# Optimization experiments

Hardware: AMD Instinct MI355X
Metric: run time of the kernel (lower is better)

## Reference

```python
import jax, jax.numpy as jnp
import numpy as np
from jax import lax

MAX_DISP = 4
KERNEL = 2 * MAX_DISP + 1  # 9
PAD = MAX_DISP             # 4


def setup_inputs() -> dict:
    key = jax.random.key(0)
    k1, k2 = jax.random.split(key)
    B, C, H, W = 4096, 512, 4, 4
    feat1 = jax.random.normal(k1, (B, C, H, W), dtype=jnp.float32)
    feat2 = jax.random.normal(k2, (B, C, H, W), dtype=jnp.float32)
    return {"feat1": feat1, "feat2": feat2}


def reference(feat1, feat2):
    # feat1, feat2: [B, C, 4, 4]
    B, C, H, W = feat1.shape
    # F.pad(feat2, [4]*4) -> [B, C, 12, 12], then crop rows/cols 2:11 -> 9x9 kernel
    feat2_pad = jnp.pad(feat2, ((0, 0), (0, 0), (PAD, PAD), (PAD, PAD)))
    feat2_crop = feat2_pad[:, :, 2:2 + KERNEL, 2:2 + KERNEL]  # [B, C, 9, 9]
    weight = feat2_crop.reshape(B * C, 1, KERNEL, KERNEL)     # OIHW, groups=B*C
    inp = feat1.reshape(1, B * C, H, W)                       # NCHW
    # torch F.conv2d is cross-correlation; lax conv is too (no kernel flip)
    corr = lax.conv_general_dilated(
        inp, weight,
        window_strides=(1, 1),
        padding=[(PAD, PAD), (PAD, PAD)],
        dimension_numbers=("NCHW", "OIHW", "NCHW"),
        feature_group_count=B * C,
    )  # [1, B*C, 4, 4]
    corr = corr.reshape(B, C, H, W)
    return corr.sum(axis=1, keepdims=True)  # [B, 1, 4, 4]
```

## Files before the change

kernel.cpp:

```cpp
#include <hip/hip_runtime.h>


__global__ __launch_bounds__(256, 4) void corr_kernel(
        const float4* __restrict__ feat1,
        const float4* __restrict__ feat2,
        float* __restrict__ out, int B) {
    const int lane  = threadIdx.x & 63;
    const int wid   = blockIdx.x * 4 + (threadIdx.x >> 6);
    const int nwave = gridDim.x * 4;

    for (int b = wid; b < B; b += nwave) {
        const size_t bbase = (size_t)b * 512;

        float4 A[2][4], W[2][4];
        {
            const size_t idx = (bbase + lane) * 4;
            #pragma unroll
            for (int i = 0; i < 4; ++i) { A[0][i] = feat1[idx + i]; W[0][i] = feat2[idx + i]; }
        }

        float acc[16];
        #pragma unroll
        for (int i = 0; i < 16; ++i) acc[i] = 0.f;

        #pragma unroll
        for (int k = 0; k < 8; ++k) {
            const int cur = k & 1, nxt = cur ^ 1;
            if (k < 7) {
                const size_t idx = (bbase + (size_t)(k + 1) * 64 + lane) * 4;
                #pragma unroll
                for (int i = 0; i < 4; ++i) { A[nxt][i] = feat1[idx + i]; W[nxt][i] = feat2[idx + i]; }
            }
            __builtin_amdgcn_sched_barrier(0);

            const float a[16] = { A[cur][0].x, A[cur][0].y, A[cur][0].z, A[cur][0].w,
                                  A[cur][1].x, A[cur][1].y, A[cur][1].z, A[cur][1].w,
                                  A[cur][2].x, A[cur][2].y, A[cur][2].z, A[cur][2].w,
                                  A[cur][3].x, A[cur][3].y, A[cur][3].z, A[cur][3].w };
            const float w[16] = { W[cur][0].x, W[cur][0].y, W[cur][0].z, W[cur][0].w,
                                  W[cur][1].x, W[cur][1].y, W[cur][1].z, W[cur][1].w,
                                  W[cur][2].x, W[cur][2].y, W[cur][2].z, W[cur][2].w,
                                  W[cur][3].x, W[cur][3].y, W[cur][3].z, W[cur][3].w };

            #pragma unroll
            for (int y = 0; y < 4; ++y)
            #pragma unroll
            for (int p = 0; p < 4; ++p) {
                const int u = y + p - 2;
                if (u < 0 || u > 3) continue;
                #pragma unroll
                for (int x = 0; x < 4; ++x)
                #pragma unroll
                for (int q = 0; q < 4; ++q) {
                    const int v = x + q - 2;
                    if (v < 0 || v > 3) continue;
                    acc[y*4 + x] = fmaf(a[u*4 + v], w[p*4 + q], acc[y*4 + x]);
                }
            }
        }

        float v[16];
        #pragma unroll
        for (int i = 0; i < 16; ++i) v[i] = acc[i];
        #pragma unroll
        for (int k = 0; k < 4; ++k) {
            const int m = 1 << k;
            const int pairs = 8 >> k;
            const bool sel = (lane >> k) & 1;
            float wtmp[8];
            #pragma unroll
            for (int p = 0; p < pairs; ++p) {
                float keep = sel ? v[2*p+1] : v[2*p];
                float send = sel ? v[2*p]   : v[2*p+1];
                float recv = __shfl_xor(send, m, 64);
                wtmp[p] = keep + recv;
            }
            #pragma unroll
            for (int p = 0; p < pairs; ++p) v[p] = wtmp[p];
        }
        float r = v[0];
        r += __shfl_xor(r, 16, 64);
        r += __shfl_xor(r, 32, 64);

        if (lane < 16) out[(size_t)b * 16 + lane] = r;
    }
}

extern "C" void kernel_launch(void* const* d_in, const int* in_sizes, int n_in,
                              void* d_out, int out_size, void* d_ws, size_t ws_size,
                              hipStream_t stream) {
    const float4* feat1 = (const float4*)d_in[0];
    const float4* feat2 = (const float4*)d_in[1];
    float* out = (float*)d_out;
    const int B = in_sizes[0] / (512 * 16);
    const int blocks = (B + 3) / 4;
    corr_kernel<<<dim3(blocks), dim3(256), 0, stream>>>(feat1, feat2, out, B);
}
```

Baseline: 271.3 us.

## Split each channel's 4x4 map across lanes using row shuffles, two waves per batch

Each lane now loads one float4 row of a channel instead of a whole 4x4 map, so lanes read consecutive 16-byte rows (coalesced). Other rows of feat2 come in through xor shuffles, cutting per-lane FMAs and register use. Each batch element is split across two waves that combine partials through shared memory, and occupancy rises to 6 blocks. This adds shuffle traffic, a block-level sync, a lane-dependent remap step before the reduction, and drops the bounds check on B.

```diff
diff --git a/kernel.cpp b/kernel.cpp
--- a/kernel.cpp
+++ b/kernel.cpp
@@ -1,88 +1,112 @@
 #include <hip/hip_runtime.h>
 
 
-__global__ __launch_bounds__(256, 4) void corr_kernel(
+__device__ __forceinline__ float4 shflx4(float4 v, int m) {
+    float4 r;
+    r.x = __shfl_xor(v.x, m, 64);
+    r.y = __shfl_xor(v.y, m, 64);
+    r.z = __shfl_xor(v.z, m, 64);
+    r.w = __shfl_xor(v.w, m, 64);
+    return r;
+}
+
+__global__ __launch_bounds__(256, 6) void corr_kernel(
         const float4* __restrict__ feat1,
         const float4* __restrict__ feat2,
-        float* __restrict__ out, int B) {
-    const int lane  = threadIdx.x & 63;
-    const int wid   = blockIdx.x * 4 + (threadIdx.x >> 6);
-    const int nwave = gridDim.x * 4;
+        float* __restrict__ out) {
+    const int tid  = threadIdx.x;
+    const int lane = tid & 63;
+    const int wv   = tid >> 6;
+    const int bsub = wv >> 1;
+    const int half = wv & 1;
+    const int b    = blockIdx.x * 2 + bsub;
+    const int u    = lane & 3;
 
-    for (int b = wid; b < B; b += nwave) {
-        const size_t bbase = (size_t)b * 512;
+    const size_t kbase = (size_t)b * 2048 + (size_t)half * 1024 + lane;
 
-        float4 A[2][4], W[2][4];
-        {
-            const size_t idx = (bbase + lane) * 4;
-            #pragma unroll
-            for (int i = 0; i < 4; ++i) { A[0][i] = feat1[idx + i]; W[0][i] = feat2[idx + i]; }
+    float racc[4][4];
+    #pragma unroll
+    for (int t = 0; t < 4; ++t)
+        #pragma unroll
+        for (int x = 0; x < 4; ++x) racc[t][x] = 0.f;
+
+    float4 Abuf[2], Wbuf[2];
+    Abuf[0] = feat1[kbase];
+    Wbuf[0] = feat2[kbase];
+
+    #pragma unroll
+    for (int j = 0; j < 16; ++j) {
+        const int cur = j & 1, nxt = cur ^ 1;
+        if (j < 15) {
+            Abuf[nxt] = feat1[kbase + (size_t)(j + 1) * 64];
+            Wbuf[nxt] = feat2[kbase + (size_t)(j + 1) * 64];
         }
+        __builtin_amdgcn_sched_barrier(0);
 
-        float acc[16];
-        #pragma unroll
-        for (int i = 0; i < 16; ++i) acc[i] = 0.f;
+        const float4 Av = Abuf[cur];
+        const float4 w0 = Wbuf[cur];
+        const float4 w1 = shflx4(w0, 1);
+        const float4 w2 = shflx4(w0, 2);
+        const float4 w3 = shflx4(w0, 3);
+
+        const float a[4] = {Av.x, Av.y, Av.z, Av.w};
+        const float wr[4][4] = {
+            {w0.x, w0.y, w0.z, w0.w},
+            {w1.x, w1.y, w1.z, w1.w},
+            {w2.x, w2.y, w2.z, w2.w},
+            {w3.x, w3.y, w3.z, w3.w}};
 
         #pragma unroll
-        for (int k = 0; k < 8; ++k) {
-            const int cur = k & 1, nxt = cur ^ 1;
-            if (k < 7) {
-                const size_t idx = (bbase + (size_t)(k + 1) * 64 + lane) * 4;
+        for (int t = 0; t < 4; ++t)
+            #pragma unroll
+            for (int x = 0; x < 4; ++x)
                 #pragma unroll
-                for (int i = 0; i < 4; ++i) { A[nxt][i] = feat1[idx + i]; W[nxt][i] = feat2[idx + i]; }
-            }
-            __builtin_amdgcn_sched_barrier(0);
+                for (int kk = 0; kk < 4; ++kk) {
+                    const int v = x + kk - 2;
+                    if (v < 0 || v > 3) continue;
+                    racc[t][x] = fmaf(a[v], wr[t][kk], racc[t][x]);
+                }
+    }
 
-            const float a[16] = { A[cur][0].x, A[cur][0].y, A[cur][0].z, A[cur][0].w,
-                                  A[cur][1].x, A[cur][1].y, A[cur][1].z, A[cur][1].w,
-                                  A[cur][2].x, A[cur][2].y, A[cur][2].z, A[cur][2].w,
-                                  A[cur][3].x, A[cur][3].y, A[cur][3].z, A[cur][3].w };
-            const float w[16] = { W[cur][0].x, W[cur][0].y, W[cur][0].z, W[cur][0].w,
-                                  W[cur][1].x, W[cur][1].y, W[cur][1].z, W[cur][1].w,
-                                  W[cur][2].x, W[cur][2].y, W[cur][2].z, W[cur][2].w,
-                                  W[cur][3].x, W[cur][3].y, W[cur][3].z, W[cur][3].w };
+    float v16[16];
+    #pragma unroll
+    for (int x = 0; x < 4; ++x) {
+        v16[2 * 4 + x] = racc[0][x];
+        v16[1 * 4 + x] = (u == 0 || u == 2) ? racc[1][x]
+                        : (u == 1 ? racc[3][x] : 0.f);
+        v16[3 * 4 + x] = (u == 1 || u == 3) ? racc[1][x]
+                        : (u == 2 ? racc[3][x] : 0.f);
+        v16[0 * 4 + x] = (u < 2) ? racc[2][x] : 0.f;
+    }
 
-            #pragma unroll
-            for (int y = 0; y < 4; ++y)
-            #pragma unroll
-            for (int p = 0; p < 4; ++p) {
-                const int u = y + p - 2;
-                if (u < 0 || u > 3) continue;
-                #pragma unroll
-                for (int x = 0; x < 4; ++x)
-                #pragma unroll
-                for (int q = 0; q < 4; ++q) {
-                    const int v = x + q - 2;
-                    if (v < 0 || v > 3) continue;
-                    acc[y*4 + x] = fmaf(a[u*4 + v], w[p*4 + q], acc[y*4 + x]);
-                }
-            }
+    #pragma unroll
+    for (int k = 0; k < 4; ++k) {
+        const int m = 1 << k;
+        const int pairs = 8 >> k;
+        const bool sel = (lane >> k) & 1;
+        float wtmp[8];
+        #pragma unroll
+        for (int p = 0; p < pairs; ++p) {
+            float keep = sel ? v16[2 * p + 1] : v16[2 * p];
+            float send = sel ? v16[2 * p]     : v16[2 * p + 1];
+            float recv = __shfl_xor(send, m, 64);
+            wtmp[p] = keep + recv;
         }
+        #pragma unroll
+        for (int p = 0; p < pairs; ++p) v16[p] = wtmp[p];
+    }
+    float r = v16[0];
+    r += __shfl_xor(r, 16, 64);
+    r += __shfl_xor(r, 32, 64);
 
-        float v[16];
-        #pragma unroll
-        for (int i = 0; i < 16; ++i) v[i] = acc[i];
-        #pragma unroll
-        for (int k = 0; k < 4; ++k) {
-            const int m = 1 << k;
-            const int pairs = 8 >> k;
-            const bool sel = (lane >> k) & 1;
-            float wtmp[8];
-            #pragma unroll
-            for (int p = 0; p < pairs; ++p) {
-                float keep = sel ? v[2*p+1] : v[2*p];
-                float send = sel ? v[2*p]   : v[2*p+1];
-                float recv = __shfl_xor(send, m, 64);
-                wtmp[p] = keep + recv;
-            }
-            #pragma unroll
-            for (int p = 0; p < pairs; ++p) v[p] = wtmp[p];
-        }
-        float r = v[0];
-        r += __shfl_xor(r, 16, 64);
-        r += __shfl_xor(r, 32, 64);
-
-        if (lane < 16) out[(size_t)b * 16 + lane] = r;
+    __shared__ float red[4][16];
+    if (lane < 16) red[wv][lane] = r;
+    __syncthreads();
+    if (tid < 32) {
+        const int bs   = tid >> 4;
+        const int comp = tid & 15;
+        const float s = red[bs * 2 + 0][comp] + red[bs * 2 + 1][comp];
+        out[(size_t)(blockIdx.x * 2 + bs) * 16 + comp] = s;
     }
 }
 
@@ -93,6 +117,5 @@
     const float4* feat2 = (const float4*)d_in[1];
     float* out = (float*)d_out;
     const int B = in_sizes[0] / (512 * 16);
-    const int blocks = (B + 3) / 4;
-    corr_kernel<<<dim3(blocks), dim3(256), 0, stream>>>(feat1, feat2, out, B);
+    corr_kernel<<<dim3(B / 2), dim3(256), 0, stream>>>(feat1, feat2, out);
 }
```

New measurement: 720.8 us. +165.7%, slower.
